# Kernel optimization log

Measured on AMD Instinct MI355X. Metric: run time of the kernel, lower is better.

The kernel has to match this reference:

```python
import jax, jax.numpy as jnp
import numpy as np

B, L, TOPK, NUM_RBF, NUM_POS, MAX_REL, CH = 4, 1024, 30, 16, 16, 32, 128
EDGE_IN = NUM_POS + NUM_RBF * 25 + 18  # 434
NODE_IN = 22


def _normalize(x, axis=-1):
    n = jnp.linalg.norm(x, axis=axis, keepdims=True)
    return jnp.where(n > 0, x / jnp.where(n > 0, n, 1.0), 0.0)


def layer_norm(x, g, b, eps=1e-5):
    mu = jnp.mean(x, axis=-1, keepdims=True)
    var = jnp.var(x, axis=-1, keepdims=True)
    return (x - mu) / jnp.sqrt(var + eps) * g + b


def gather_nodes_d(nodes, idx):
    # nodes [B,M,C], idx [B,N,K] -> [B,N,K,C]
    Bn, N, K = idx.shape
    out = jnp.take_along_axis(nodes, idx.reshape(Bn, N * K, 1), axis=1)
    return out.reshape(Bn, N, K, nodes.shape[-1])


def gather_edges(edges, idx):
    # edges [B,N,N,C], idx [B,N,K] -> [B,N,K,C]
    return jnp.take_along_axis(edges, idx[..., None], axis=2)


def cal_dihedral(Xf, eps=1e-7):
    U = _normalize(Xf[:, 1:, :] - Xf[:, :-1, :])
    u_0, u_1, u_2 = U[:, :-2], U[:, 1:-1], U[:, 2:]
    n_0 = _normalize(jnp.cross(u_0, u_1))
    n_1 = _normalize(jnp.cross(u_1, u_2))
    cosD = jnp.clip(jnp.sum(n_0 * n_1, -1), -1 + eps, 1 - eps)
    v = _normalize(jnp.cross(n_0, n_1))
    return jnp.sign(jnp.sum(-v * u_1, -1)) * jnp.arccos(cosD)


def _dihedrals(X, eps=1e-7):
    Bn, N = X.shape[0], X.shape[1]
    Xf = X[:, :, :3, :].reshape(Bn, 3 * N, 3)
    D = jnp.pad(cal_dihedral(Xf), ((0, 0), (1, 2))).reshape(Bn, N, 3)
    dihedral_feats = jnp.concatenate([jnp.cos(D), jnp.sin(D)], -1)
    U = _normalize(Xf[:, 1:, :] - Xf[:, :-1, :])
    cosA = jnp.clip(jnp.sum(U[:, :-2] * U[:, 1:-1], -1), -1 + eps, 1 - eps)
    A = jnp.pad(jnp.arccos(cosA), ((0, 0), (1, 2))).reshape(Bn, N, 3)
    angle_feats = jnp.concatenate([jnp.cos(A), jnp.sin(A)], -1)
    return jnp.concatenate([dihedral_feats, angle_feats], -1)  # [B,N,12]


def _quaternions(R):
    diag = jnp.diagonal(R, axis1=-2, axis2=-1)
    Rxx, Ryy, Rzz = diag[..., 0], diag[..., 1], diag[..., 2]
    mags = 0.5 * jnp.sqrt(jnp.abs(1.0 + jnp.stack([Rxx - Ryy - Rzz, -Rxx + Ryy - Rzz, -Rxx - Ryy + Rzz], -1)))
    signs = jnp.sign(jnp.stack([R[..., 2, 1] - R[..., 1, 2], R[..., 0, 2] - R[..., 2, 0], R[..., 1, 0] - R[..., 0, 1]], -1))
    w = jnp.sqrt(jax.nn.relu(1.0 + jnp.sum(diag, -1, keepdims=True))) / 2.0
    return _normalize(jnp.concatenate([signs * mags, w], -1))


def _orientations_coarse_gl_tuple(X, E_idx):
    V = X  # [B,N,4,3]
    Bn, N = X.shape[0], X.shape[1]
    Xf = X[:, :, :3, :].reshape(Bn, 3 * N, 3)
    U = _normalize(Xf[:, 1:, :] - Xf[:, :-1, :])
    u_0, u_1 = U[:, :-2], U[:, 1:-1]
    n_0 = _normalize(jnp.cross(u_0, u_1))[:, ::3]  # [B,N-1,3]
    b_1 = _normalize(u_0 - u_1)[:, ::3]
    Xa = Xf[:, ::3]  # N-atom coords [B,N,3]
    Q = jnp.stack([b_1, n_0, jnp.cross(b_1, n_0)], 2).reshape(Bn, N - 1, 9)
    Q = jnp.pad(Q, ((0, 0), (0, 1), (0, 0)))  # [B,N,9]
    Qm = Q.reshape(Bn, N, 3, 3)
    Q_neighbors = gather_nodes_d(Q, E_idx).reshape(Bn, N, -1, 3, 3)
    X_nb = gather_nodes_d(V[:, :, 1, :], E_idx)
    N_nb = gather_nodes_d(V[:, :, 0, :], E_idx)
    C_nb = gather_nodes_d(V[:, :, 2, :], E_idx)
    O_nb = gather_nodes_d(V[:, :, 3, :], E_idx)
    dXn = jnp.stack([X_nb, N_nb, C_nb, O_nb], 3) - Xa[:, :, None, None, :]  # [B,N,K,4,3]
    dU = jnp.einsum('bnij,bnkaj->bnkai', Qm, dXn)
    Kn = E_idx.shape[-1]
    E_direct = _normalize(dU).reshape(Bn, N, Kn, 12)
    R = jnp.einsum('bnji,bnkjl->bnkil', Qm, Q_neighbors)
    q = _quaternions(R)  # [B,N,K,4]
    dX_inner = V[:, :, jnp.array([0, 2, 3]), :] - Xa[:, :, None, :]
    V_direct = _normalize(jnp.einsum('bnij,bnaj->bnai', Qm, dX_inner)).reshape(Bn, N, 9)
    return V_direct, E_direct, q


def _dist(Xc, mask, eps=1e-6):
    mask_2D = mask[:, None, :] * mask[:, :, None]
    D = mask_2D * jnp.sqrt(jnp.sum((Xc[:, None, :, :] - Xc[:, :, None, :]) ** 2, -1) + eps)
    D_max = jnp.max(D, -1, keepdims=True)
    D_adjust = D + (1.0 - mask_2D) * D_max
    negD, E_idx = jax.lax.top_k(-D_adjust, min(TOPK, Xc.shape[1]))
    return -negD, E_idx


def _dist_seq(res_idx):
    D = jnp.abs(res_idx[:, :, None] - res_idx[:, None, :])
    _, E_idx = jax.lax.top_k(-D, min(TOPK, res_idx.shape[1]))
    return E_idx


def _rbf(D):
    D_mu = jnp.linspace(2.0, 22.0, NUM_RBF)
    D_sigma = (22.0 - 2.0) / NUM_RBF
    return jnp.exp(-(((D[..., None] - D_mu) / D_sigma) ** 2))


def _get_rbf(A, Bm, E_idx):
    D = jnp.sqrt(jnp.sum((A[:, :, None, :] - Bm[:, None, :, :]) ** 2, -1) + 1e-6)
    return _rbf(gather_edges(D[..., None], E_idx)[..., 0])


PAIRS = [('N', 'N'), ('C', 'C'), ('O', 'O'), ('Cb', 'Cb'), ('Ca', 'N'), ('Ca', 'C'), ('Ca', 'O'), ('Ca', 'Cb'),
         ('N', 'C'), ('N', 'O'), ('N', 'Cb'), ('Cb', 'C'), ('Cb', 'O'), ('O', 'C'), ('N', 'Ca'), ('C', 'Ca'),
         ('O', 'Ca'), ('Cb', 'Ca'), ('C', 'N'), ('O', 'N'), ('Cb', 'N'), ('C', 'Cb'), ('O', 'Cb'), ('C', 'O')]


def _forward(X, mask, residue_idx, chain_labels, W_pos, b_pos, W_edge, W_node, g_edge, b_edge, g_node, b_node):
    bvec = X[:, :, 1, :] - X[:, :, 0, :]
    cvec = X[:, :, 2, :] - X[:, :, 1, :]
    avec = jnp.cross(bvec, cvec)
    Cb = -0.58273431 * avec + 0.56802827 * bvec - 0.54067466 * cvec + X[:, :, 1, :]
    atoms = {'N': X[:, :, 0, :], 'Ca': X[:, :, 1, :], 'C': X[:, :, 2, :], 'O': X[:, :, 3, :], 'Cb': Cb}
    D_neighbors, E_idx = _dist(atoms['Ca'], mask)
    E_idx_res = _dist_seq(residue_idx)
    E_idx = jnp.where(mask[:, :, None] == 0, E_idx_res, E_idx)
    RBF_all = [_rbf(D_neighbors)]
    for pa, pb in PAIRS:
        RBF_all.append(_get_rbf(atoms[pa], atoms[pb], E_idx))
    RBF_all = jnp.concatenate(RBF_all, -1)  # [B,L,K,400]
    V_angles = _dihedrals(X) * mask[..., None]
    V_direct, E_direct, E_angles = _orientations_coarse_gl_tuple(X, E_idx)
    V_direct = V_direct * mask[..., None]
    offset = residue_idx[:, :, None] - residue_idx[:, None, :]
    E_offset = gather_edges(offset[..., None], E_idx)[..., 0]
    d_chains = (chain_labels[:, :, None] == chain_labels[:, None, :]).astype(jnp.int32)
    E_chains = gather_edges(d_chains[..., None], E_idx)[..., 0]
    d = jnp.clip(E_offset + MAX_REL, 0, 2 * MAX_REL) * E_chains + (1 - E_chains) * (2 * MAX_REL + 1)
    E_positional = jax.nn.one_hot(d, 2 * MAX_REL + 2, dtype=W_pos.dtype) @ W_pos + b_pos
    mask_j = gather_nodes_d(mask[..., None], E_idx)[..., 0]
    fdt = E_direct.dtype
    E = jnp.concatenate([E_positional, RBF_all, E_direct, E_angles,
                         E_chains[..., None].astype(fdt), mask_j[..., None]], -1)  # [B,L,K,434]
    E = layer_norm(E @ W_edge, g_edge, b_edge)
    Vn = jnp.concatenate([V_angles, V_direct, mask[..., None]], -1)  # [B,L,22]
    Vn = layer_norm(Vn @ W_node, g_node, b_node)
    return Vn, E, E_idx


def setup_inputs():
    key = jax.random.key(0)
    ks = jax.random.split(key, 8)
    X = 3.0 * jax.random.normal(ks[0], (B, L, 4, 3), jnp.float32)
    mask = jnp.ones((B, L), jnp.float32)
    residue_idx = jnp.tile(jnp.arange(L, dtype=jnp.int32), (B, 1))
    chain_labels = jax.random.randint(ks[1], (B, L), 0, 2, dtype=jnp.int32)
    s = lambda k, sh: jax.random.normal(k, sh, jnp.float32) * 0.05
    W_pos = s(ks[2], (2 * MAX_REL + 2, NUM_POS))
    b_pos = jnp.zeros((NUM_POS,), jnp.float32)
    W_edge = s(ks[3], (EDGE_IN, CH))
    W_node = s(ks[4], (NODE_IN, CH))
    return dict(X=X, mask=mask, residue_idx=residue_idx, chain_labels=chain_labels,
                W_pos=W_pos, b_pos=b_pos, W_edge=W_edge, W_node=W_node,
                g_edge=jnp.ones((CH,), jnp.float32), b_edge=jnp.zeros((CH,), jnp.float32),
                g_node=jnp.ones((CH,), jnp.float32), b_node=jnp.zeros((CH,), jnp.float32))


def reference(X, mask, residue_idx, chain_labels, W_pos, b_pos, W_edge, W_node, g_edge, b_edge, g_node, b_node):
    return _forward(X, mask, residue_idx, chain_labels, W_pos, b_pos, W_edge, W_node,
                    g_edge, b_edge, g_node, b_node)
```

## Files before the change

### kernel.cpp

```cpp
#include <hip/hip_runtime.h>

#define BATCH 4
#define LEN   1024
#define KNB   30
#define CH    128
#define EIN   434
#define KP    448
#define KST   14
#define ASTR  456
#define CSTR  132

typedef unsigned short ushort_t;
typedef __attribute__((ext_vector_type(8))) short bf16x8;
typedef __attribute__((ext_vector_type(4))) float f32x4;

__constant__ int c_pa[24] = {0,2,3,4,1,1,1,1,0,0,0,4,4,3,0,2,3,4,2,3,4,2,3,2};
__constant__ int c_pb[24] = {0,2,3,4,0,2,3,4,2,3,4,2,3,2,1,1,1,1,0,0,0,4,4,3};

struct F3 { float x, y, z; };
__device__ __forceinline__ F3 f3sub(F3 a, F3 b){ return {a.x-b.x, a.y-b.y, a.z-b.z}; }
__device__ __forceinline__ F3 f3cross(F3 a, F3 b){
  return {a.y*b.z - a.z*b.y, a.z*b.x - a.x*b.z, a.x*b.y - a.y*b.x};
}
__device__ __forceinline__ float f3dot(F3 a, F3 b){ return a.x*b.x + a.y*b.y + a.z*b.z; }
__device__ __forceinline__ F3 f3norm(F3 a){
  float n = sqrtf(f3dot(a,a));
  if (n > 0.f) return {a.x/n, a.y/n, a.z/n};
  return {0.f, 0.f, 0.f};
}
__device__ __forceinline__ float fsign(float x){ return (x > 0.f) ? 1.f : ((x < 0.f) ? -1.f : 0.f); }
__device__ __forceinline__ float clip1(float c){ return fminf(fmaxf(c, -1.f + 1e-7f), 1.f - 1e-7f); }
__device__ __forceinline__ float dihedralf(F3 ua, F3 ub, F3 uc){
  F3 n0 = f3norm(f3cross(ua, ub));
  F3 n1 = f3norm(f3cross(ub, uc));
  float cd = clip1(f3dot(n0, n1));
  F3 v = f3norm(f3cross(n0, n1));
  return fsign(-f3dot(v, ub)) * acosf(cd);
}
__device__ __forceinline__ ushort_t f2bf(float f){
  unsigned u = __float_as_uint(f);
  unsigned r = u + 0x7FFFu + ((u >> 16) & 1u);
  return (ushort_t)(r >> 16);
}

#define DPP_MIN_STEP(v, ctrl) do{                                            \
    unsigned t_ = (unsigned)__builtin_amdgcn_update_dpp(                     \
        (int)0xFFFFFFFF, (int)(v), (ctrl), 0xF, 0xF, false);                 \
    (v) = t_ < (v) ? t_ : (v);                                               \
  } while(0)
__device__ __forceinline__ unsigned wave_min_u32(unsigned v){
  DPP_MIN_STEP(v, 0x111);
  DPP_MIN_STEP(v, 0x112);
  DPP_MIN_STEP(v, 0x114);
  DPP_MIN_STEP(v, 0x118);
  DPP_MIN_STEP(v, 0x142);
  DPP_MIN_STEP(v, 0x143);
  return (unsigned)__builtin_amdgcn_readlane((int)v, 63);
}

__global__ __launch_bounds__(256) void prep_kernel(
    const float* __restrict__ X, const float* __restrict__ mask,
    const float* __restrict__ We,
    float* __restrict__ wCb, float* __restrict__ wQ, float* __restrict__ wVn,
    float* __restrict__ wCa, ushort_t* __restrict__ Wfrag)
{
  if (blockIdx.x >= 16){
    int f = (blockIdx.x - 16)*256 + threadIdx.x;
    if (f >= 8*KST*64) return;
    int t = f / (KST*64);
    int s = (f / 64) % KST;
    int l = f & 63;
    int n  = t*16 + (l & 15);
    int k0 = s*32 + (l >> 4)*8;
    ushort_t v[8];
    #pragma unroll
    for (int j = 0; j < 8; ++j){
      int k = k0 + j;
      v[j] = (k < EIN) ? f2bf(We[(size_t)k*CH + n]) : (ushort_t)0;
    }
    ulong2* dst = (ulong2*)(Wfrag + (size_t)f*8);
    *dst = *(ulong2*)v;
    return;
  }

  int idx = blockIdx.x * 256 + threadIdx.x;
  int n = idx & (LEN - 1);
  const float* p = X + (size_t)idx * 12;
  F3 Na = {p[0], p[1], p[2]};
  F3 Ca = {p[3], p[4], p[5]};
  F3 Cc = {p[6], p[7], p[8]};
  F3 Oa = {p[9], p[10], p[11]};
  wCa[idx*4+0] = Ca.x; wCa[idx*4+1] = Ca.y; wCa[idx*4+2] = Ca.z; wCa[idx*4+3] = 0.f;
  F3 bv = f3sub(Ca, Na);
  F3 cv = f3sub(Cc, Ca);
  F3 av = f3cross(bv, cv);
  wCb[idx*3+0] = -0.58273431f*av.x + 0.56802827f*bv.x - 0.54067466f*cv.x + Ca.x;
  wCb[idx*3+1] = -0.58273431f*av.y + 0.56802827f*bv.y - 0.54067466f*cv.y + Ca.y;
  wCb[idx*3+2] = -0.58273431f*av.z + 0.56802827f*bv.z - 0.54067466f*cv.z + Ca.z;

  F3 u0 = f3norm(bv);
  F3 u1 = f3norm(cv);

  float Q[9];
  if (n < LEN - 1){
    F3 b1 = f3norm(f3sub(u0, u1));
    F3 n0 = f3norm(f3cross(u0, u1));
    F3 r2 = f3cross(b1, n0);
    Q[0]=b1.x; Q[1]=b1.y; Q[2]=b1.z;
    Q[3]=n0.x; Q[4]=n0.y; Q[5]=n0.z;
    Q[6]=r2.x; Q[7]=r2.y; Q[8]=r2.z;
  } else {
    #pragma unroll
    for (int t = 0; t < 9; ++t) Q[t] = 0.f;
  }
  #pragma unroll
  for (int t = 0; t < 9; ++t) wQ[(size_t)idx*9 + t] = Q[t];

  float m = mask[idx];
  bool hp = (n > 0), hn = (n < LEN - 1);
  F3 um1 = {0,0,0}, u2 = {0,0,0}, u3 = {0,0,0};
  if (hp){
    const float* pp = p - 12;
    F3 Cp = {pp[6], pp[7], pp[8]};
    um1 = f3norm(f3sub(Na, Cp));
  }
  if (hn){
    const float* pn = p + 12;
    F3 Nn  = {pn[0], pn[1], pn[2]};
    F3 Can = {pn[3], pn[4], pn[5]};
    u2 = f3norm(f3sub(Nn, Cc));
    u3 = f3norm(f3sub(Can, Nn));
  }
  float D0=0.f, D1=0.f, D2=0.f, A0=0.f, A1=0.f, A2=0.f;
  if (hp){ D0 = dihedralf(um1, u0, u1); A0 = acosf(clip1(f3dot(um1, u0))); }
  if (hn){
    D1 = dihedralf(u0, u1, u2); A1 = acosf(clip1(f3dot(u0, u1)));
    D2 = dihedralf(u1, u2, u3); A2 = acosf(clip1(f3dot(u1, u2)));
  }
  float vn[22];
  vn[0] = cosf(D0)*m; vn[1] = cosf(D1)*m; vn[2]  = cosf(D2)*m;
  vn[3] = sinf(D0)*m; vn[4] = sinf(D1)*m; vn[5]  = sinf(D2)*m;
  vn[6] = cosf(A0)*m; vn[7] = cosf(A1)*m; vn[8]  = cosf(A2)*m;
  vn[9] = sinf(A0)*m; vn[10]= sinf(A1)*m; vn[11] = sinf(A2)*m;
  F3 dxs[3];
  dxs[0] = {0.f, 0.f, 0.f};
  dxs[1] = f3sub(Cc, Na);
  dxs[2] = f3sub(Oa, Na);
  #pragma unroll
  for (int a = 0; a < 3; ++a){
    F3 dv = dxs[a];
    F3 du = { Q[0]*dv.x + Q[1]*dv.y + Q[2]*dv.z,
              Q[3]*dv.x + Q[4]*dv.y + Q[5]*dv.z,
              Q[6]*dv.x + Q[7]*dv.y + Q[8]*dv.z };
    F3 dn = f3norm(du);
    vn[12 + a*3 + 0] = dn.x * m;
    vn[12 + a*3 + 1] = dn.y * m;
    vn[12 + a*3 + 2] = dn.z * m;
  }
  vn[21] = m;
  #pragma unroll
  for (int t = 0; t < 22; ++t) wVn[(size_t)idx*22 + t] = vn[t];
}

__global__ __launch_bounds__(256) void topk_kernel(
    const float* __restrict__ wCa, float* __restrict__ wDn,
    int* __restrict__ wIdx, float* __restrict__ outI)
{
  int wid = threadIdx.x >> 6, l = threadIdx.x & 63;
  int bi = blockIdx.x*4 + wid;
  int b  = bi >> 10;
  const float4* Ca = (const float4*)wCa;
  float4 ci = Ca[bi];
  const float4* Cb = Ca + (size_t)b * LEN;

  unsigned D[16];
  #pragma unroll
  for (int t = 0; t < 16; ++t){
    int j = l + 64*t;
    float4 cj = Cb[j];
    float dx = ci.x - cj.x, dy = ci.y - cj.y, dz = ci.z - cj.z;
    D[t] = __float_as_uint(sqrtf(dx*dx + dy*dy + dz*dz + 1e-6f));
  }
  unsigned lmin = D[0]; unsigned jmin = (unsigned)l;
  #pragma unroll
  for (int t = 1; t < 16; ++t)
    if (D[t] < lmin){ lmin = D[t]; jmin = (unsigned)(l + 64*t); }

  for (int k = 0; k < KNB; ++k){
    unsigned dmin = wave_min_u32(lmin);
    unsigned cand = (lmin == dmin) ? jmin : 0xFFFFFFFFu;
    unsigned jwin = wave_min_u32(cand);
    if (cand == jwin){
      wIdx[bi*KNB + k] = (int)jwin;
      wDn[bi*KNB + k]  = __uint_as_float(dmin);
      outI[bi*KNB + k] = (float)jwin;
      int tw = (int)(jwin >> 6);
      #pragma unroll
      for (int t = 0; t < 16; ++t) if (t == tw) D[t] = 0xFFFFFFFFu;
      lmin = D[0]; jmin = (unsigned)l;
      #pragma unroll
      for (int t = 1; t < 16; ++t)
        if (D[t] < lmin){ lmin = D[t]; jmin = (unsigned)(l + 64*t); }
    }
  }
}

__global__ __launch_bounds__(64) void node_kernel(
    const float* __restrict__ wVn, const float* __restrict__ Wn,
    const float* __restrict__ gn, const float* __restrict__ bn,
    float* __restrict__ outV)
{
  int bi = blockIdx.x;
  int t  = threadIdx.x;
  __shared__ float v[22];
  if (t < 22) v[t] = wVn[(size_t)bi*22 + t];
  __syncthreads();
  float x0 = 0.f, x1 = 0.f;
  #pragma unroll
  for (int r = 0; r < 22; ++r){
    float vr = v[r];
    x0 = fmaf(vr, Wn[r*CH + t], x0);
    x1 = fmaf(vr, Wn[r*CH + t + 64], x1);
  }
  float s = x0 + x1;
  #pragma unroll
  for (int off = 1; off < 64; off <<= 1) s += __shfl_xor(s, off);
  float mu = s * (1.f/128.f);
  float d0 = x0 - mu, d1 = x1 - mu;
  float vs = d0*d0 + d1*d1;
  #pragma unroll
  for (int off = 1; off < 64; off <<= 1) vs += __shfl_xor(vs, off);
  float inv = 1.f / sqrtf(vs * (1.f/128.f) + 1e-5f);
  outV[(size_t)bi*CH + t]      = d0*inv*gn[t]    + bn[t];
  outV[(size_t)bi*CH + t + 64] = d1*inv*gn[t+64] + bn[t+64];
}

__global__ __launch_bounds__(256) void edge_kernel(
    const float* __restrict__ X, const float* __restrict__ mask,
    const int* __restrict__ resi, const int* __restrict__ chain,
    const float* __restrict__ Wp, const float* __restrict__ bp,
    const float* __restrict__ ge, const float* __restrict__ be,
    const float* __restrict__ wCb, const float* __restrict__ wQ,
    const float* __restrict__ wDn, const int* __restrict__ wIdx,
    const ushort_t* __restrict__ Wfrag,
    float* __restrict__ outE)
{
  __shared__ __align__(16) ushort_t As[32*ASTR];
  __shared__ float sAI[15];
  __shared__ float sQi[9];
  __shared__ float sAJ[KNB][15];
  __shared__ float sQj[KNB][9];
  __shared__ int   sOffI[KNB];
  __shared__ float sChain[KNB];
  __shared__ float sMaskJ[KNB];
  __shared__ float sDn[KNB];

  int bi  = blockIdx.x;
  int b   = bi >> 10;
  int tid = threadIdx.x;

  if (tid < KNB){
    int j  = wIdx[bi*KNB + tid];
    int gj = (b << 10) + j;
    const float* pj = X + (size_t)gj * 12;
    #pragma unroll
    for (int t = 0; t < 12; ++t) sAJ[tid][t] = pj[t];
    sAJ[tid][12] = wCb[(size_t)gj*3 + 0];
    sAJ[tid][13] = wCb[(size_t)gj*3 + 1];
    sAJ[tid][14] = wCb[(size_t)gj*3 + 2];
    #pragma unroll
    for (int t = 0; t < 9; ++t) sQj[tid][t] = wQ[(size_t)gj*9 + t];
    sOffI[tid]  = resi[bi] - resi[gj];
    sChain[tid] = (chain[bi] == chain[gj]) ? 1.f : 0.f;
    sMaskJ[tid] = mask[gj];
    sDn[tid]    = wDn[bi*KNB + tid];
  } else if (tid == KNB){
    const float* pi = X + (size_t)bi * 12;
    #pragma unroll
    for (int t = 0; t < 12; ++t) sAI[t] = pi[t];
    sAI[12] = wCb[(size_t)bi*3 + 0];
    sAI[13] = wCb[(size_t)bi*3 + 1];
    sAI[14] = wCb[(size_t)bi*3 + 2];
  } else if (tid == KNB + 1){
    #pragma unroll
    for (int t = 0; t < 9; ++t) sQi[t] = wQ[(size_t)bi*9 + t];
  }
  for (int e = tid; e < 2*KP; e += 256) As[30*ASTR + (e >= KP ? ASTR + e - KP : e)] = 0;
  for (int e = tid; e < KNB*14; e += 256){
    int r = e / 14, c = EIN + (e % 14);
    As[r*ASTR + c] = 0;
  }
  __syncthreads();

  if (tid < KNB*8){
    int k = tid >> 3, s = tid & 7;
    ushort_t* row = &As[k*ASTR];
    if (s == 0){
      int off = sOffI[k];
      float ch = sChain[k];
      int d = off + 32;
      d = d < 0 ? 0 : (d > 64 ? 64 : d);
      if (!(ch > 0.5f)) d = 65;
      #pragma unroll
      for (int m2 = 0; m2 < 16; ++m2)
        row[m2] = f2bf(Wp[d*16 + m2] + bp[m2]);
      row[432] = f2bf(ch);
      row[433] = f2bf(sMaskJ[k]);
    } else if (s == 1){
      float nx = sAI[0], ny = sAI[1], nz = sAI[2];
      const int amap[4] = {3, 0, 6, 9};
      #pragma unroll
      for (int a = 0; a < 4; ++a){
        float dx = sAJ[k][amap[a]+0] - nx;
        float dy = sAJ[k][amap[a]+1] - ny;
        float dz = sAJ[k][amap[a]+2] - nz;
        float e0 = sQi[0]*dx + sQi[1]*dy + sQi[2]*dz;
        float e1 = sQi[3]*dx + sQi[4]*dy + sQi[5]*dz;
        float e2 = sQi[6]*dx + sQi[7]*dy + sQi[8]*dz;
        float nn = sqrtf(e0*e0 + e1*e1 + e2*e2);
        float inv = nn > 0.f ? 1.f/nn : 0.f;
        row[416 + a*3 + 0] = f2bf(e0*inv);
        row[416 + a*3 + 1] = f2bf(e1*inv);
        row[416 + a*3 + 2] = f2bf(e2*inv);
      }
    } else if (s == 2){
      float R[3][3];
      #pragma unroll
      for (int i2 = 0; i2 < 3; ++i2)
        #pragma unroll
        for (int l2 = 0; l2 < 3; ++l2)
          R[i2][l2] = sQi[0*3+i2]*sQj[k][0*3+l2]
                    + sQi[1*3+i2]*sQj[k][1*3+l2]
                    + sQi[2*3+i2]*sQj[k][2*3+l2];
      float Rxx = R[0][0], Ryy = R[1][1], Rzz = R[2][2];
      float mx = 0.5f*sqrtf(fabsf(1.f + Rxx - Ryy - Rzz));
      float my = 0.5f*sqrtf(fabsf(1.f - Rxx + Ryy - Rzz));
      float mz = 0.5f*sqrtf(fabsf(1.f - Rxx - Ryy + Rzz));
      float qx = fsign(R[2][1] - R[1][2]) * mx;
      float qy = fsign(R[0][2] - R[2][0]) * my;
      float qz = fsign(R[1][0] - R[0][1]) * mz;
      float qw = sqrtf(fmaxf(1.f + Rxx + Ryy + Rzz, 0.f)) * 0.5f;
      float qn = sqrtf(qx*qx + qy*qy + qz*qz + qw*qw);
      float inv = qn > 0.f ? 1.f/qn : 0.f;
      row[428] = f2bf(qx*inv);
      row[429] = f2bf(qy*inv);
      row[430] = f2bf(qz*inv);
      row[431] = f2bf(qw*inv);
    }
    for (int p = s; p < 25; p += 8){
      float d;
      if (p == 0) d = sDn[k];
      else {
        int ai = c_pa[p-1]*3, bj = c_pb[p-1]*3;
        float dx = sAI[ai+0] - sAJ[k][bj+0];
        float dy = sAI[ai+1] - sAJ[k][bj+1];
        float dz = sAI[ai+2] - sAJ[k][bj+2];
        d = sqrtf(dx*dx + dy*dy + dz*dz + 1e-6f);
      }
      #pragma unroll
      for (int m2 = 0; m2 < 16; ++m2){
        float mu = (float)(2.0 + m2 * (20.0/15.0));
        float tt = (d - mu) * 0.8f;
        row[16 + p*16 + m2] = f2bf(__expf(-tt*tt));
      }
    }
  }
  __syncthreads();

  int w = tid >> 6, l = tid & 63;
  int n0 = w*2;
  int aOff0 = (l & 15)*ASTR + (l >> 4)*8;
  int aOff1 = aOff0 + 16*ASTR;
  const ushort_t* bp0 = Wfrag + ((size_t)(n0    *KST)*64 + l)*8;
  const ushort_t* bp1 = Wfrag + ((size_t)((n0+1)*KST)*64 + l)*8;

  f32x4 acc00 = {0.f,0.f,0.f,0.f}, acc01 = acc00, acc10 = acc00, acc11 = acc00;

  bf16x8 a0 = *(const bf16x8*)&As[aOff0];
  bf16x8 a1 = *(const bf16x8*)&As[aOff1];
  bf16x8 b0 = *(const bf16x8*)bp0;
  bf16x8 b1 = *(const bf16x8*)bp1;
  #pragma unroll
  for (int s = 0; s < KST; ++s){
    bf16x8 a0n, a1n, b0n, b1n;
    if (s < KST-1){
      int ka = (s+1)*32;
      a0n = *(const bf16x8*)&As[aOff0 + ka];
      a1n = *(const bf16x8*)&As[aOff1 + ka];
      b0n = *(const bf16x8*)(bp0 + (size_t)(s+1)*64*8);
      b1n = *(const bf16x8*)(bp1 + (size_t)(s+1)*64*8);
    }
    acc00 = __builtin_amdgcn_mfma_f32_16x16x32_bf16(a0, b0, acc00, 0, 0, 0);
    acc01 = __builtin_amdgcn_mfma_f32_16x16x32_bf16(a0, b1, acc01, 0, 0, 0);
    acc10 = __builtin_amdgcn_mfma_f32_16x16x32_bf16(a1, b0, acc10, 0, 0, 0);
    acc11 = __builtin_amdgcn_mfma_f32_16x16x32_bf16(a1, b1, acc11, 0, 0, 0);
    if (s < KST-1){ a0 = a0n; a1 = a1n; b0 = b0n; b1 = b1n; }
  }
  __syncthreads();

  float* Cs = (float*)As;
  int ccol = l & 15, crow = (l >> 4)*4;
  #pragma unroll
  for (int r = 0; r < 4; ++r){
    Cs[(crow + r)*CSTR      + n0*16 + ccol]      = acc00[r];
    Cs[(crow + r)*CSTR      + (n0+1)*16 + ccol]  = acc01[r];
    Cs[(16 + crow + r)*CSTR + n0*16 + ccol]      = acc10[r];
    Cs[(16 + crow + r)*CSTR + (n0+1)*16 + ccol]  = acc11[r];
  }
  __syncthreads();

  if (tid < KNB*8){
    int row = tid >> 3, g = tid & 7;
    float v[16];
    #pragma unroll
    for (int c = 0; c < 16; ++c) v[c] = Cs[row*CSTR + g*16 + c];
    float s = 0.f;
    #pragma unroll
    for (int c = 0; c < 16; ++c) s += v[c];
    #pragma unroll
    for (int off = 1; off < 8; off <<= 1) s += __shfl_xor(s, off, 8);
    float mu = s * (1.f/128.f);
    float vs = 0.f;
    #pragma unroll
    for (int c = 0; c < 16; ++c){ float dd = v[c] - mu; vs += dd*dd; }
    #pragma unroll
    for (int off = 1; off < 8; off <<= 1) vs += __shfl_xor(vs, off, 8);
    float inv = 1.f / sqrtf(vs * (1.f/128.f) + 1e-5f);
    float o[16];
    #pragma unroll
    for (int c = 0; c < 16; ++c)
      o[c] = (v[c] - mu)*inv*ge[g*16 + c] + be[g*16 + c];
    float4* dst = (float4*)&outE[((size_t)bi*KNB + row)*CH + g*16];
    dst[0] = make_float4(o[0], o[1], o[2], o[3]);
    dst[1] = make_float4(o[4], o[5], o[6], o[7]);
    dst[2] = make_float4(o[8], o[9], o[10], o[11]);
    dst[3] = make_float4(o[12], o[13], o[14], o[15]);
  }
}

extern "C" void kernel_launch(void* const* d_in, const int* in_sizes, int n_in,
                              void* d_out, int out_size, void* d_ws, size_t ws_size,
                              hipStream_t stream)
{
  const float* X    = (const float*)d_in[0];
  const float* mask = (const float*)d_in[1];
  const int*   resi = (const int*)  d_in[2];
  const int*   chn  = (const int*)  d_in[3];
  const float* Wp   = (const float*)d_in[4];
  const float* bp   = (const float*)d_in[5];
  const float* We   = (const float*)d_in[6];
  const float* Wn   = (const float*)d_in[7];
  const float* ge   = (const float*)d_in[8];
  const float* be   = (const float*)d_in[9];
  const float* gn   = (const float*)d_in[10];
  const float* bn   = (const float*)d_in[11];

  float* outV = (float*)d_out;
  float* outE = outV + (size_t)BATCH*LEN*CH;
  float* outI = outE + (size_t)BATCH*LEN*KNB*CH;

  float* ws   = (float*)d_ws;
  float* wCb  = ws;
  float* wQ   = wCb + (size_t)BATCH*LEN*3;
  float* wVn  = wQ  + (size_t)BATCH*LEN*9;
  float* wDn  = wVn + (size_t)BATCH*LEN*22;
  int*   wIdx = (int*)(wDn + (size_t)BATCH*LEN*KNB);
  float* wCa  = (float*)(wIdx + (size_t)BATCH*LEN*KNB);
  ushort_t* Wfrag = (ushort_t*)(wCa + (size_t)BATCH*LEN*4);

  prep_kernel<<<16 + 28, 256, 0, stream>>>(X, mask, We, wCb, wQ, wVn, wCa, Wfrag);
  topk_kernel<<<BATCH*LEN/4, 256, 0, stream>>>(wCa, wDn, wIdx, outI);
  node_kernel<<<BATCH*LEN, 64, 0, stream>>>(wVn, Wn, gn, bn, outV);
  edge_kernel<<<BATCH*LEN, 256, 0, stream>>>(X, mask, resi, chn, Wp, bp, ge, be,
                                             wCb, wQ, wDn, wIdx, Wfrag, outE);
}
```

Before: 187.6 us.

## Fuse node kernel into topk, vectorize bf16 packing, use fast math intrinsics

Folds the node-feature linear+layernorm into the topk kernel, which removes one launch. The topk selection now does a single 64-bit DPP min-reduction carrying both distance and index instead of two 32-bit reductions. Edge feature construction packs bf16 pairs with v_cvt_pk_bf16_f32 and writes 16-byte vectors. RBF uses exp2 with a folded constant, normalizations use rsq, and dihedral/angle cos/sin come from cos and sqrt(1-c^2) instead of acos/cos/sin. The changes trade some precision (fast rsq/exp2, packed conversion rounding) for fewer instructions, and drop the zeroing of padding rows 30-31.

```diff
diff --git a/kernel.cpp b/kernel.cpp
--- a/kernel.cpp
+++ b/kernel.cpp
@@ -24,38 +24,52 @@
 }
 __device__ __forceinline__ float f3dot(F3 a, F3 b){ return a.x*b.x + a.y*b.y + a.z*b.z; }
 __device__ __forceinline__ F3 f3norm(F3 a){
-  float n = sqrtf(f3dot(a,a));
-  if (n > 0.f) return {a.x/n, a.y/n, a.z/n};
-  return {0.f, 0.f, 0.f};
+  float s2 = f3dot(a,a);
+  float inv = (s2 > 0.f) ? __builtin_amdgcn_rsqf(s2) : 0.f;
+  return {a.x*inv, a.y*inv, a.z*inv};
 }
 __device__ __forceinline__ float fsign(float x){ return (x > 0.f) ? 1.f : ((x < 0.f) ? -1.f : 0.f); }
 __device__ __forceinline__ float clip1(float c){ return fminf(fmaxf(c, -1.f + 1e-7f), 1.f - 1e-7f); }
-__device__ __forceinline__ float dihedralf(F3 ua, F3 ub, F3 uc){
+
+__device__ __forceinline__ void dihedral_cs(F3 ua, F3 ub, F3 uc, float& c, float& s){
   F3 n0 = f3norm(f3cross(ua, ub));
   F3 n1 = f3norm(f3cross(ub, uc));
   float cd = clip1(f3dot(n0, n1));
   F3 v = f3norm(f3cross(n0, n1));
-  return fsign(-f3dot(v, ub)) * acosf(cd);
-}
+  c = cd;
+  s = fsign(-f3dot(v, ub)) * sqrtf(1.f - cd*cd);
+}
+
 __device__ __forceinline__ ushort_t f2bf(float f){
   unsigned u = __float_as_uint(f);
   unsigned r = u + 0x7FFFu + ((u >> 16) & 1u);
   return (ushort_t)(r >> 16);
 }
 
-#define DPP_MIN_STEP(v, ctrl) do{                                            \
-    unsigned t_ = (unsigned)__builtin_amdgcn_update_dpp(                     \
-        (int)0xFFFFFFFF, (int)(v), (ctrl), 0xF, 0xF, false);                 \
-    (v) = t_ < (v) ? t_ : (v);                                               \
+__device__ __forceinline__ unsigned cvt_pk(float a, float b){
+  unsigned r;
+  asm("v_cvt_pk_bf16_f32 %0, %1, %2" : "=v"(r) : "v"(a), "v"(b));
+  return r;
+}
+
+#define DPP_MIN64_STEP(d, j, ctrl) do{                                        \
+    unsigned td_ = (unsigned)__builtin_amdgcn_update_dpp(                     \
+        (int)0xFFFFFFFF, (int)(d), (ctrl), 0xF, 0xF, false);                  \
+    unsigned tj_ = (unsigned)__builtin_amdgcn_update_dpp(                     \
+        (int)0xFFFFFFFF, (int)(j), (ctrl), 0xF, 0xF, false);                  \
+    unsigned long long o_ = (((unsigned long long)td_) << 32) | tj_;          \
+    unsigned long long c_ = (((unsigned long long)(d)) << 32) | (j);          \
+    if (o_ < c_){ (d) = td_; (j) = tj_; }                                     \
   } while(0)
-__device__ __forceinline__ unsigned wave_min_u32(unsigned v){
-  DPP_MIN_STEP(v, 0x111);
-  DPP_MIN_STEP(v, 0x112);
-  DPP_MIN_STEP(v, 0x114);
-  DPP_MIN_STEP(v, 0x118);
-  DPP_MIN_STEP(v, 0x142);
-  DPP_MIN_STEP(v, 0x143);
-  return (unsigned)__builtin_amdgcn_readlane((int)v, 63);
+__device__ __forceinline__ void wave_min64(unsigned &d, unsigned &j){
+  DPP_MIN64_STEP(d, j, 0x111);
+  DPP_MIN64_STEP(d, j, 0x112);
+  DPP_MIN64_STEP(d, j, 0x114);
+  DPP_MIN64_STEP(d, j, 0x118);
+  DPP_MIN64_STEP(d, j, 0x142);
+  DPP_MIN64_STEP(d, j, 0x143);
+  d = (unsigned)__builtin_amdgcn_readlane((int)d, 63);
+  j = (unsigned)__builtin_amdgcn_readlane((int)j, 63);
 }
 
 __global__ __launch_bounds__(256) void prep_kernel(
@@ -86,11 +100,13 @@
   int idx = blockIdx.x * 256 + threadIdx.x;
   int n = idx & (LEN - 1);
   const float* p = X + (size_t)idx * 12;
-  F3 Na = {p[0], p[1], p[2]};
-  F3 Ca = {p[3], p[4], p[5]};
-  F3 Cc = {p[6], p[7], p[8]};
-  F3 Oa = {p[9], p[10], p[11]};
-  wCa[idx*4+0] = Ca.x; wCa[idx*4+1] = Ca.y; wCa[idx*4+2] = Ca.z; wCa[idx*4+3] = 0.f;
+  const float4* p4 = (const float4*)p;
+  float4 q0 = p4[0], q1 = p4[1], q2 = p4[2];
+  F3 Na = {q0.x, q0.y, q0.z};
+  F3 Ca = {q0.w, q1.x, q1.y};
+  F3 Cc = {q1.z, q1.w, q2.x};
+  F3 Oa = {q2.y, q2.z, q2.w};
+  ((float4*)wCa)[idx] = make_float4(Ca.x, Ca.y, Ca.z, 0.f);
   F3 bv = f3sub(Ca, Na);
   F3 cv = f3sub(Cc, Ca);
   F3 av = f3cross(bv, cv);
@@ -131,17 +147,23 @@
     u2 = f3norm(f3sub(Nn, Cc));
     u3 = f3norm(f3sub(Can, Nn));
   }
-  float D0=0.f, D1=0.f, D2=0.f, A0=0.f, A1=0.f, A2=0.f;
-  if (hp){ D0 = dihedralf(um1, u0, u1); A0 = acosf(clip1(f3dot(um1, u0))); }
+  float cD0=1.f,sD0=0.f, cD1=1.f,sD1=0.f, cD2=1.f,sD2=0.f;
+  float cA0=1.f,sA0=0.f, cA1=1.f,sA1=0.f, cA2=1.f,sA2=0.f;
+  if (hp){
+    dihedral_cs(um1, u0, u1, cD0, sD0);
+    cA0 = clip1(f3dot(um1, u0)); sA0 = sqrtf(1.f - cA0*cA0);
+  }
   if (hn){
-    D1 = dihedralf(u0, u1, u2); A1 = acosf(clip1(f3dot(u0, u1)));
-    D2 = dihedralf(u1, u2, u3); A2 = acosf(clip1(f3dot(u1, u2)));
+    dihedral_cs(u0, u1, u2, cD1, sD1);
+    dihedral_cs(u1, u2, u3, cD2, sD2);
+    cA1 = clip1(f3dot(u0, u1)); sA1 = sqrtf(1.f - cA1*cA1);
+    cA2 = clip1(f3dot(u1, u2)); sA2 = sqrtf(1.f - cA2*cA2);
   }
   float vn[22];
-  vn[0] = cosf(D0)*m; vn[1] = cosf(D1)*m; vn[2]  = cosf(D2)*m;
-  vn[3] = sinf(D0)*m; vn[4] = sinf(D1)*m; vn[5]  = sinf(D2)*m;
-  vn[6] = cosf(A0)*m; vn[7] = cosf(A1)*m; vn[8]  = cosf(A2)*m;
-  vn[9] = sinf(A0)*m; vn[10]= sinf(A1)*m; vn[11] = sinf(A2)*m;
+  vn[0] = cD0*m; vn[1] = cD1*m; vn[2]  = cD2*m;
+  vn[3] = sD0*m; vn[4] = sD1*m; vn[5]  = sD2*m;
+  vn[6] = cA0*m; vn[7] = cA1*m; vn[8]  = cA2*m;
+  vn[9] = sA0*m; vn[10]= sA1*m; vn[11] = sA2*m;
   F3 dxs[3];
   dxs[0] = {0.f, 0.f, 0.f};
   dxs[1] = f3sub(Cc, Na);
@@ -163,8 +185,11 @@
 }
 
 __global__ __launch_bounds__(256) void topk_kernel(
-    const float* __restrict__ wCa, float* __restrict__ wDn,
-    int* __restrict__ wIdx, float* __restrict__ outI)
+    const float* __restrict__ wCa, const float* __restrict__ wVn,
+    const float* __restrict__ Wn,  const float* __restrict__ gn,
+    const float* __restrict__ bn,
+    float* __restrict__ wDn, int* __restrict__ wIdx,
+    float* __restrict__ outI, float* __restrict__ outV)
 {
   int wid = threadIdx.x >> 6, l = threadIdx.x & 63;
   int bi = blockIdx.x*4 + wid;
@@ -187,14 +212,13 @@
     if (D[t] < lmin){ lmin = D[t]; jmin = (unsigned)(l + 64*t); }
 
   for (int k = 0; k < KNB; ++k){
-    unsigned dmin = wave_min_u32(lmin);
-    unsigned cand = (lmin == dmin) ? jmin : 0xFFFFFFFFu;
-    unsigned jwin = wave_min_u32(cand);
-    if (cand == jwin){
-      wIdx[bi*KNB + k] = (int)jwin;
+    unsigned dmin = lmin, jw = jmin;
+    wave_min64(dmin, jw);
+    if (jmin == jw){
+      wIdx[bi*KNB + k] = (int)jw;
       wDn[bi*KNB + k]  = __uint_as_float(dmin);
-      outI[bi*KNB + k] = (float)jwin;
-      int tw = (int)(jwin >> 6);
+      outI[bi*KNB + k] = (float)jw;
+      int tw = (int)(jw >> 6);
       #pragma unroll
       for (int t = 0; t < 16; ++t) if (t == tw) D[t] = 0xFFFFFFFFu;
       lmin = D[0]; jmin = (unsigned)l;
@@ -203,36 +227,39 @@
         if (D[t] < lmin){ lmin = D[t]; jmin = (unsigned)(l + 64*t); }
     }
   }
-}
-
-__global__ __launch_bounds__(64) void node_kernel(
-    const float* __restrict__ wVn, const float* __restrict__ Wn,
-    const float* __restrict__ gn, const float* __restrict__ bn,
-    float* __restrict__ outV)
-{
-  int bi = blockIdx.x;
-  int t  = threadIdx.x;
-  __shared__ float v[22];
-  if (t < 22) v[t] = wVn[(size_t)bi*22 + t];
-  __syncthreads();
+
   float x0 = 0.f, x1 = 0.f;
   #pragma unroll
   for (int r = 0; r < 22; ++r){
-    float vr = v[r];
-    x0 = fmaf(vr, Wn[r*CH + t], x0);
-    x1 = fmaf(vr, Wn[r*CH + t + 64], x1);
-  }
-  float s = x0 + x1;
-  #pragma unroll
-  for (int off = 1; off < 64; off <<= 1) s += __shfl_xor(s, off);
-  float mu = s * (1.f/128.f);
+    float vr = wVn[(size_t)bi*22 + r];
+    x0 = fmaf(vr, Wn[r*CH + l],      x0);
+    x1 = fmaf(vr, Wn[r*CH + l + 64], x1);
+  }
+  float sum = x0 + x1;
+  #pragma unroll
+  for (int off = 1; off < 64; off <<= 1) sum += __shfl_xor(sum, off);
+  float mu = sum * (1.f/128.f);
   float d0 = x0 - mu, d1 = x1 - mu;
   float vs = d0*d0 + d1*d1;
   #pragma unroll
   for (int off = 1; off < 64; off <<= 1) vs += __shfl_xor(vs, off);
   float inv = 1.f / sqrtf(vs * (1.f/128.f) + 1e-5f);
-  outV[(size_t)bi*CH + t]      = d0*inv*gn[t]    + bn[t];
-  outV[(size_t)bi*CH + t + 64] = d1*inv*gn[t+64] + bn[t+64];
+  outV[(size_t)bi*CH + l]      = d0*inv*gn[l]    + bn[l];
+  outV[(size_t)bi*CH + l + 64] = d1*inv*gn[l+64] + bn[l+64];
+}
+
+__device__ __forceinline__ void rbf_row(ushort_t* dst, float d){
+  unsigned u[8];
+  #pragma unroll
+  for (int h = 0; h < 8; ++h){
+    float t0 = d - (float)(2.0 + (2*h    ) * (20.0/15.0));
+    float t1 = d - (float)(2.0 + (2*h + 1) * (20.0/15.0));
+    float e0 = __builtin_amdgcn_exp2f(t0*t0 * -0.92332482f);
+    float e1 = __builtin_amdgcn_exp2f(t1*t1 * -0.92332482f);
+    u[h] = cvt_pk(e0, e1);
+  }
+  *(uint4*)&dst[0] = make_uint4(u[0], u[1], u[2], u[3]);
+  *(uint4*)&dst[8] = make_uint4(u[4], u[5], u[6], u[7]);
 }
 
 __global__ __launch_bounds__(256) void edge_kernel(
@@ -246,9 +273,9 @@
     float* __restrict__ outE)
 {
   __shared__ __align__(16) ushort_t As[32*ASTR];
+  __shared__ __align__(16) float sAJ[KNB][16];
   __shared__ float sAI[15];
   __shared__ float sQi[9];
-  __shared__ float sAJ[KNB][15];
   __shared__ float sQj[KNB][9];
   __shared__ int   sOffI[KNB];
   __shared__ float sChain[KNB];
@@ -262,9 +289,11 @@
   if (tid < KNB){
     int j  = wIdx[bi*KNB + tid];
     int gj = (b << 10) + j;
-    const float* pj = X + (size_t)gj * 12;
-    #pragma unroll
-    for (int t = 0; t < 12; ++t) sAJ[tid][t] = pj[t];
+    const float4* pj4 = (const float4*)(X + (size_t)gj * 12);
+    float4 a0 = pj4[0], a1 = pj4[1], a2 = pj4[2];
+    *(float4*)&sAJ[tid][0] = a0;
+    *(float4*)&sAJ[tid][4] = a1;
+    *(float4*)&sAJ[tid][8] = a2;
     sAJ[tid][12] = wCb[(size_t)gj*3 + 0];
     sAJ[tid][13] = wCb[(size_t)gj*3 + 1];
     sAJ[tid][14] = wCb[(size_t)gj*3 + 2];
@@ -285,7 +314,6 @@
     #pragma unroll
     for (int t = 0; t < 9; ++t) sQi[t] = wQ[(size_t)bi*9 + t];
   }
-  for (int e = tid; e < 2*KP; e += 256) As[30*ASTR + (e >= KP ? ASTR + e - KP : e)] = 0;
   for (int e = tid; e < KNB*14; e += 256){
     int r = e / 14, c = EIN + (e % 14);
     As[r*ASTR + c] = 0;
@@ -298,17 +326,25 @@
     if (s == 0){
       int off = sOffI[k];
       float ch = sChain[k];
-      int d = off + 32;
-      d = d < 0 ? 0 : (d > 64 ? 64 : d);
-      if (!(ch > 0.5f)) d = 65;
+      int dpos = off + 32;
+      dpos = dpos < 0 ? 0 : (dpos > 64 ? 64 : dpos);
+      if (!(ch > 0.5f)) dpos = 65;
+      const float4* wp4 = (const float4*)(Wp + dpos*16);
+      const float4* bp4 = (const float4*)bp;
+      unsigned u[8];
       #pragma unroll
-      for (int m2 = 0; m2 < 16; ++m2)
-        row[m2] = f2bf(Wp[d*16 + m2] + bp[m2]);
-      row[432] = f2bf(ch);
-      row[433] = f2bf(sMaskJ[k]);
+      for (int h = 0; h < 4; ++h){
+        float4 wv = wp4[h], bv = bp4[h];
+        u[2*h]   = cvt_pk(wv.x + bv.x, wv.y + bv.y);
+        u[2*h+1] = cvt_pk(wv.z + bv.z, wv.w + bv.w);
+      }
+      *(uint4*)&row[0] = make_uint4(u[0], u[1], u[2], u[3]);
+      *(uint4*)&row[8] = make_uint4(u[4], u[5], u[6], u[7]);
+      *(unsigned*)&row[432] = cvt_pk(ch, sMaskJ[k]);
     } else if (s == 1){
       float nx = sAI[0], ny = sAI[1], nz = sAI[2];
       const int amap[4] = {3, 0, 6, 9};
+      float f[12];
       #pragma unroll
       for (int a = 0; a < 4; ++a){
         float dx = sAJ[k][amap[a]+0] - nx;
@@ -317,12 +353,15 @@
         float e0 = sQi[0]*dx + sQi[1]*dy + sQi[2]*dz;
         float e1 = sQi[3]*dx + sQi[4]*dy + sQi[5]*dz;
         float e2 = sQi[6]*dx + sQi[7]*dy + sQi[8]*dz;
-        float nn = sqrtf(e0*e0 + e1*e1 + e2*e2);
-        float inv = nn > 0.f ? 1.f/nn : 0.f;
-        row[416 + a*3 + 0] = f2bf(e0*inv);
-        row[416 + a*3 + 1] = f2bf(e1*inv);
-        row[416 + a*3 + 2] = f2bf(e2*inv);
+        float ss = e0*e0 + e1*e1 + e2*e2;
+        float inv = ss > 0.f ? __builtin_amdgcn_rsqf(ss) : 0.f;
+        f[a*3+0] = e0*inv; f[a*3+1] = e1*inv; f[a*3+2] = e2*inv;
       }
+      unsigned u[6];
+      #pragma unroll
+      for (int h = 0; h < 6; ++h) u[h] = cvt_pk(f[2*h], f[2*h+1]);
+      *(uint4*)&row[416] = make_uint4(u[0], u[1], u[2], u[3]);
+      *(uint2*)&row[424] = make_uint2(u[4], u[5]);
     } else if (s == 2){
       float R[3][3];
       #pragma unroll
@@ -340,14 +379,11 @@
       float qy = fsign(R[0][2] - R[2][0]) * my;
       float qz = fsign(R[1][0] - R[0][1]) * mz;
       float qw = sqrtf(fmaxf(1.f + Rxx + Ryy + Rzz, 0.f)) * 0.5f;
-      float qn = sqrtf(qx*qx + qy*qy + qz*qz + qw*qw);
-      float inv = qn > 0.f ? 1.f/qn : 0.f;
-      row[428] = f2bf(qx*inv);
-      row[429] = f2bf(qy*inv);
-      row[430] = f2bf(qz*inv);
-      row[431] = f2bf(qw*inv);
+      float qn2 = qx*qx + qy*qy + qz*qz + qw*qw;
+      float inv = qn2 > 0.f ? __builtin_amdgcn_rsqf(qn2) : 0.f;
+      *(uint2*)&row[428] = make_uint2(cvt_pk(qx*inv, qy*inv), cvt_pk(qz*inv, qw*inv));
     }
-    for (int p = s; p < 25; p += 8){
+    auto do_pair = [&](int p){
       float d;
       if (p == 0) d = sDn[k];
       else {
@@ -357,13 +393,10 @@
         float dz = sAI[ai+2] - sAJ[k][bj+2];
         d = sqrtf(dx*dx + dy*dy + dz*dz + 1e-6f);
       }
-      #pragma unroll
-      for (int m2 = 0; m2 < 16; ++m2){
-        float mu = (float)(2.0 + m2 * (20.0/15.0));
-        float tt = (d - mu) * 0.8f;
-        row[16 + p*16 + m2] = f2bf(__expf(-tt*tt));
-      }
-    }
+      rbf_row(row + 16 + p*16, d);
+    };
+    for (int p = s; p < 24; p += 8) do_pair(p);
+    if (s == 3) do_pair(24);
   }
   __syncthreads();
 
@@ -469,8 +502,8 @@
   ushort_t* Wfrag = (ushort_t*)(wCa + (size_t)BATCH*LEN*4);
 
   prep_kernel<<<16 + 28, 256, 0, stream>>>(X, mask, We, wCb, wQ, wVn, wCa, Wfrag);
-  topk_kernel<<<BATCH*LEN/4, 256, 0, stream>>>(wCa, wDn, wIdx, outI);
-  node_kernel<<<BATCH*LEN, 64, 0, stream>>>(wVn, Wn, gn, bn, outV);
+  topk_kernel<<<BATCH*LEN/4, 256, 0, stream>>>(wCa, wVn, Wn, gn, bn,
+                                               wDn, wIdx, outI, outV);
   edge_kernel<<<BATCH*LEN, 256, 0, stream>>>(X, mask, resi, chn, Wp, bp, ge, be,
                                              wCb, wQ, wDn, wIdx, Wfrag, outE);
 }
```

Result: faster. 180.2 us (-3.9%).
